# Kernel optimization log

Measured on AMD Instinct MI355X. Metric: run time of the kernel, lower is better.

The kernel has to match this reference:

```python
import jax, jax.numpy as jnp
import numpy as np

EPS = 1e-6

def _grad_magnitude(x):
    # x: [B, 1, D, H, W]. Valid 3x3x3 conv with shift-subtract kernels:
    # kernel_w differences along D, kernel_d along H, kernel_h along W.
    g_w = x[:, :, 2:, 1:-1, 1:-1] - x[:, :, :-2, 1:-1, 1:-1]
    g_d = x[:, :, 1:-1, 2:, 1:-1] - x[:, :, 1:-1, :-2, 1:-1]
    g_h = x[:, :, 1:-1, 1:-1, 2:] - x[:, :, 1:-1, 1:-1, :-2]
    mag = jnp.sqrt(g_w * g_w + g_d * g_d + g_h * g_h + EPS)
    # replicate-pad back to original spatial size
    return jnp.pad(mag, ((0, 0), (0, 0), (1, 1), (1, 1), (1, 1)), mode='edge')

def setup_inputs() -> dict:
    key = jax.random.key(0)
    k1, k2 = jax.random.split(key)
    shape = (1, 1, 256, 256, 256)
    x1 = jax.random.normal(k1, shape, dtype=jnp.float32)
    x2 = jax.random.normal(k2, shape, dtype=jnp.float32)
    return {"x1": x1, "x2": x2}

def reference(x1, x2):
    g1 = _grad_magnitude(x1)
    g2 = _grad_magnitude(x2)
    return jnp.mean(jnp.abs(g1 - g2))
```

## Files before the change

### kernel.cpp

```cpp
#include <hip/hip_runtime.h>


#define D_CHUNK 4

__global__ __launch_bounds__(256) void grad_loss_kernel(const float* __restrict__ xf1,
                                                        const float* __restrict__ xf2,
                                                        double* __restrict__ acc) {
    const float4* __restrict__ x1 = (const float4*)xf1;
    const float4* __restrict__ x2 = (const float4*)xf2;

    __shared__ float4 plane[2][2][6][64];

    const int tid   = threadIdx.x;
    const int lane  = tid & 63;
    const int wid   = tid >> 6;
    const int htile = blockIdx.x & 63;
    const int dchk  = blockIdx.x >> 6;

    const int h0 = 1 + htile * 4;
    const int d0 = 1 + dchk * D_CHUNK;

    const int  h    = h0 + wid;
    const bool live = (h <= 254);
    const int  hrow = (h <= 255) ? h : 255;

    const int halo_row  = (wid < 2) ? (h0 - 1) : ((h0 + 4 <= 255) ? (h0 + 4) : 255);
    const int halo_slot = (wid < 2) ? 0 : 5;
    const int halo_inp  = wid & 1;
    const float4* __restrict__ halo4 = halo_inp ? x2 : x1;

    const int own_f4  = hrow * 64 + lane;
    const int halo_f4 = halo_row * 64 + lane;

    const float ww0 = (lane == 0)  ? 0.0f : 1.0f;
    const float ww1 = (lane == 0)  ? 2.0f : 1.0f;
    const float ww2 = (lane == 63) ? 2.0f : 1.0f;
    const float ww3 = (lane == 63) ? 0.0f : 1.0f;
    const float whf = (h == 1 || h == 254) ? 2.0f : 1.0f;

    float4 a1 = x1[(d0 - 1) * 16384 + own_f4];
    float4 a2 = x2[(d0 - 1) * 16384 + own_f4];
    float4 b1 = x1[d0 * 16384 + own_f4];
    float4 b2 = x2[d0 * 16384 + own_f4];
    float4 hb = halo4[d0 * 16384 + halo_f4];
    float4 c1 = x1[(d0 + 1) * 16384 + own_f4];
    float4 c2 = x2[(d0 + 1) * 16384 + own_f4];
    float4 hc = halo4[(d0 + 1) * 16384 + halo_f4];

    plane[0][0][wid + 1][lane] = b1;
    plane[0][1][wid + 1][lane] = b2;
    plane[0][halo_inp][halo_slot][lane] = hb;
    __syncthreads();

    float val = 0.0f;

    #pragma unroll
    for (int i = 0; i < D_CHUNK; ++i) {
        const int d   = d0 + i;
        const int cur = i & 1;
        const int nxt = cur ^ 1;
        const int dn  = (d + 2 <= 255) ? (d + 2) : 255;

        float4 n1 = x1[dn * 16384 + own_f4];
        float4 n2 = x2[dn * 16384 + own_f4];
        float4 hn = halo4[dn * 16384 + halo_f4];

        plane[nxt][0][wid + 1][lane] = c1;
        plane[nxt][1][wid + 1][lane] = c2;
        plane[nxt][halo_inp][halo_slot][lane] = hc;

        if (live && d <= 254) {
            float4 u1 = plane[cur][0][wid][lane];
            float4 v1 = plane[cur][0][wid + 2][lane];
            float4 u2 = plane[cur][1][wid][lane];
            float4 v2 = plane[cur][1][wid + 2][lane];

            float l1 = __shfl_up(b1.w, 1, 64);
            float r1 = __shfl_down(b1.x, 1, 64);
            float l2 = __shfl_up(b2.w, 1, 64);
            float r2 = __shfl_down(b2.x, 1, 64);

            float gw, gd, gh;
            gw = c1.x - a1.x; gd = v1.x - u1.x; gh = b1.y - l1;
            float m10 = __builtin_amdgcn_sqrtf(gw * gw + gd * gd + gh * gh + 1e-6f);
            gw = c1.y - a1.y; gd = v1.y - u1.y; gh = b1.z - b1.x;
            float m11 = __builtin_amdgcn_sqrtf(gw * gw + gd * gd + gh * gh + 1e-6f);
            gw = c1.z - a1.z; gd = v1.z - u1.z; gh = b1.w - b1.y;
            float m12 = __builtin_amdgcn_sqrtf(gw * gw + gd * gd + gh * gh + 1e-6f);
            gw = c1.w - a1.w; gd = v1.w - u1.w; gh = r1 - b1.z;
            float m13 = __builtin_amdgcn_sqrtf(gw * gw + gd * gd + gh * gh + 1e-6f);

            gw = c2.x - a2.x; gd = v2.x - u2.x; gh = b2.y - l2;
            float m20 = __builtin_amdgcn_sqrtf(gw * gw + gd * gd + gh * gh + 1e-6f);
            gw = c2.y - a2.y; gd = v2.y - u2.y; gh = b2.z - b2.x;
            float m21 = __builtin_amdgcn_sqrtf(gw * gw + gd * gd + gh * gh + 1e-6f);
            gw = c2.z - a2.z; gd = v2.z - u2.z; gh = b2.w - b2.y;
            float m22 = __builtin_amdgcn_sqrtf(gw * gw + gd * gd + gh * gh + 1e-6f);
            gw = c2.w - a2.w; gd = v2.w - u2.w; gh = r2 - b2.z;
            float m23 = __builtin_amdgcn_sqrtf(gw * gw + gd * gd + gh * gh + 1e-6f);

            float inner = ww0 * fabsf(m10 - m20)
                        + ww1 * fabsf(m11 - m21)
                        + ww2 * fabsf(m12 - m22)
                        + ww3 * fabsf(m13 - m23);

            const float wdf = (d == 1 || d == 254) ? 2.0f : 1.0f;
            val += wdf * whf * inner;
        }

        a1 = b1; b1 = c1; c1 = n1;
        a2 = b2; b2 = c2; c2 = n2;
        hc = hn;
        __syncthreads();
    }

    for (int off = 32; off > 0; off >>= 1)
        val += __shfl_down(val, off, 64);

    __shared__ float smem[4];
    if (lane == 0) smem[wid] = val;
    __syncthreads();

    if (wid == 0) {
        float s = (lane < 4) ? smem[lane] : 0.0f;
        s += __shfl_down(s, 2, 64);
        s += __shfl_down(s, 1, 64);
        if (lane == 0)
            atomicAdd(&acc[blockIdx.x & 255], (double)s);
    }
}

__global__ void finalize_kernel(const double* __restrict__ acc, float* __restrict__ out) {
    double v = acc[threadIdx.x];
    for (int off = 32; off > 0; off >>= 1)
        v += __shfl_down(v, off, 64);

    __shared__ double smem[4];
    const int lid = threadIdx.x & 63;
    const int wid = threadIdx.x >> 6;
    if (lid == 0) smem[wid] = v;
    __syncthreads();

    if (threadIdx.x == 0) {
        double s = smem[0] + smem[1] + smem[2] + smem[3];
        out[0] = (float)(s / 16777216.0);
    }
}

extern "C" void kernel_launch(void* const* d_in, const int* in_sizes, int n_in,
                              void* d_out, int out_size, void* d_ws, size_t ws_size,
                              hipStream_t stream) {
    const float* x1 = (const float*)d_in[0];
    const float* x2 = (const float*)d_in[1];
    float* out = (float*)d_out;
    double* acc = (double*)d_ws;

    hipMemsetAsync(d_ws, 0, 256 * sizeof(double), stream);
    grad_loss_kernel<<<64 * 64, 256, 0, stream>>>(x1, x2, acc);
    finalize_kernel<<<1, 256, 0, stream>>>(acc, out);
}
```

Baseline: 147.1 us.

## Double H-tile per block to 8 rows and use DPP for lateral neighbor shifts

```diff
diff --git a/kernel.cpp b/kernel.cpp
--- a/kernel.cpp
+++ b/kernel.cpp
@@ -3,30 +3,40 @@
 
 #define D_CHUNK 4
 
-__global__ __launch_bounds__(256) void grad_loss_kernel(const float* __restrict__ xf1,
-                                                        const float* __restrict__ xf2,
-                                                        double* __restrict__ acc) {
+__device__ __forceinline__ float dpp_shl1(float x) {
+    return __int_as_float(__builtin_amdgcn_update_dpp(
+        0, __float_as_int(x), 0x130, 0xF, 0xF, true));
+}
+__device__ __forceinline__ float dpp_shr1(float x) {
+    return __int_as_float(__builtin_amdgcn_update_dpp(
+        0, __float_as_int(x), 0x138, 0xF, 0xF, true));
+}
+
+__global__ __launch_bounds__(512, 8) void grad_loss_kernel(const float* __restrict__ xf1,
+                                                           const float* __restrict__ xf2,
+                                                           double* __restrict__ acc) {
     const float4* __restrict__ x1 = (const float4*)xf1;
     const float4* __restrict__ x2 = (const float4*)xf2;
 
-    __shared__ float4 plane[2][2][6][64];
+    __shared__ float4 plane[2][2][10][64];
 
     const int tid   = threadIdx.x;
     const int lane  = tid & 63;
     const int wid   = tid >> 6;
-    const int htile = blockIdx.x & 63;
-    const int dchk  = blockIdx.x >> 6;
+    const int htile = blockIdx.x & 31;
+    const int dchk  = blockIdx.x >> 5;
 
-    const int h0 = 1 + htile * 4;
+    const int h0 = 1 + htile * 8;
     const int d0 = 1 + dchk * D_CHUNK;
 
     const int  h    = h0 + wid;
     const bool live = (h <= 254);
     const int  hrow = (h <= 255) ? h : 255;
 
-    const int halo_row  = (wid < 2) ? (h0 - 1) : ((h0 + 4 <= 255) ? (h0 + 4) : 255);
-    const int halo_slot = (wid < 2) ? 0 : 5;
-    const int halo_inp  = wid & 1;
+    const bool has_halo  = (wid < 2) || (wid > 5);
+    const int  halo_row  = (wid < 2) ? (h0 - 1) : ((h0 + 8 <= 255) ? (h0 + 8) : 255);
+    const int  halo_slot = (wid < 2) ? 0 : 9;
+    const int  halo_inp  = wid & 1;
     const float4* __restrict__ halo4 = halo_inp ? x2 : x1;
 
     const int own_f4  = hrow * 64 + lane;
@@ -42,14 +52,17 @@
     float4 a2 = x2[(d0 - 1) * 16384 + own_f4];
     float4 b1 = x1[d0 * 16384 + own_f4];
     float4 b2 = x2[d0 * 16384 + own_f4];
-    float4 hb = halo4[d0 * 16384 + halo_f4];
     float4 c1 = x1[(d0 + 1) * 16384 + own_f4];
     float4 c2 = x2[(d0 + 1) * 16384 + own_f4];
-    float4 hc = halo4[(d0 + 1) * 16384 + halo_f4];
+    float4 hb = make_float4(0, 0, 0, 0), hc = hb;
+    if (has_halo) {
+        hb = halo4[d0 * 16384 + halo_f4];
+        hc = halo4[(d0 + 1) * 16384 + halo_f4];
+    }
 
     plane[0][0][wid + 1][lane] = b1;
     plane[0][1][wid + 1][lane] = b2;
-    plane[0][halo_inp][halo_slot][lane] = hb;
+    if (has_halo) plane[0][halo_inp][halo_slot][lane] = hb;
     __syncthreads();
 
     float val = 0.0f;
@@ -63,11 +76,12 @@
 
         float4 n1 = x1[dn * 16384 + own_f4];
         float4 n2 = x2[dn * 16384 + own_f4];
-        float4 hn = halo4[dn * 16384 + halo_f4];
+        float4 hn = make_float4(0, 0, 0, 0);
+        if (has_halo) hn = halo4[dn * 16384 + halo_f4];
 
         plane[nxt][0][wid + 1][lane] = c1;
         plane[nxt][1][wid + 1][lane] = c2;
-        plane[nxt][halo_inp][halo_slot][lane] = hc;
+        if (has_halo) plane[nxt][halo_inp][halo_slot][lane] = hc;
 
         if (live && d <= 254) {
             float4 u1 = plane[cur][0][wid][lane];
@@ -75,10 +89,10 @@
             float4 u2 = plane[cur][1][wid][lane];
             float4 v2 = plane[cur][1][wid + 2][lane];
 
-            float l1 = __shfl_up(b1.w, 1, 64);
-            float r1 = __shfl_down(b1.x, 1, 64);
-            float l2 = __shfl_up(b2.w, 1, 64);
-            float r2 = __shfl_down(b2.x, 1, 64);
+            float l1 = dpp_shl1(b1.w);
+            float r1 = dpp_shr1(b1.x);
+            float l2 = dpp_shl1(b2.w);
+            float r2 = dpp_shr1(b2.x);
 
             float gw, gd, gh;
             gw = c1.x - a1.x; gd = v1.x - u1.x; gh = b1.y - l1;
@@ -117,12 +131,13 @@
     for (int off = 32; off > 0; off >>= 1)
         val += __shfl_down(val, off, 64);
 
-    __shared__ float smem[4];
-    if (lane == 0) smem[wid] = val;
+    float* red = (float*)&plane[0][0][0][0];
+    if (lane == 0) red[wid] = val;
     __syncthreads();
 
     if (wid == 0) {
-        float s = (lane < 4) ? smem[lane] : 0.0f;
+        float s = (lane < 8) ? red[lane] : 0.0f;
+        s += __shfl_down(s, 4, 64);
         s += __shfl_down(s, 2, 64);
         s += __shfl_down(s, 1, 64);
         if (lane == 0)
@@ -156,6 +171,6 @@
     double* acc = (double*)d_ws;
 
     hipMemsetAsync(d_ws, 0, 256 * sizeof(double), stream);
-    grad_loss_kernel<<<64 * 64, 256, 0, stream>>>(x1, x2, acc);
+    grad_loss_kernel<<<32 * 64, 512, 0, stream>>>(x1, x2, acc);
     finalize_kernel<<<1, 256, 0, stream>>>(acc, out);
 }
```

Measured after the change: 204.0 us. +38.7%, slower.
